# Kernel optimization log

Hardware: AMD Instinct MI355X
Metric: run time of the kernel (lower is better)

## Reference

```python
import jax, jax.numpy as jnp
import numpy as np

GROUP_SIZE = 128
HIDDEN = 2048
INTER = 5632
TOKENS = 8192
_SHIFTS = jnp.arange(8, dtype=jnp.uint32) * 4  # 4-bit nibbles, 8 per int32


def _pack_rows(nib):
    # nib: [in, out] int values in [0,16); pack 8 consecutive rows into one int32
    r, c = nib.shape
    n = nib.reshape(r // 8, 8, c).astype(jnp.uint32)
    packed = jnp.sum(n << _SHIFTS[None, :, None], axis=1, dtype=jnp.uint32)
    return jax.lax.bitcast_convert_type(packed, jnp.int32)  # [in//8, out]


def _pack_cols(nib):
    # nib: [groups, out]; pack 8 consecutive cols into one int32
    g, o = nib.shape
    n = nib.reshape(g, o // 8, 8).astype(jnp.uint32)
    packed = jnp.sum(n << _SHIFTS[None, None, :], axis=-1, dtype=jnp.uint32)
    return jax.lax.bitcast_convert_type(packed, jnp.int32)  # [groups, out//8]


def _dequant(qweight, qzeros, scales, group_size=GROUP_SIZE):
    # GPTQ int4 dequant: w = (q - (z + 1)) * scale, per group of `group_size` input rows
    in_packed, out = qweight.shape
    in_dim = in_packed * 8
    groups = scales.shape[0]
    sh = jnp.arange(8, dtype=jnp.int32) * 4
    q = (qweight[:, None, :] >> sh[None, :, None]) & 0xF       # [in//8, 8, out]
    q = q.reshape(in_dim, out)
    z = (qzeros[:, :, None] >> sh[None, None, :]) & 0xF        # [groups, out//8, 8]
    z = z.reshape(groups, out)
    gidx = jnp.arange(in_dim) // group_size                    # [in]
    w = (q - (z[gidx] + 1)).astype(scales.dtype) * scales[gidx]
    return w  # [in, out]


def setup_inputs() -> dict:
    key = jax.random.key(0)
    ks = jax.random.split(key, 10)
    x = jax.random.normal(ks[0], (TOKENS, HIDDEN), dtype=jnp.float32)

    def make(kq, kz, ksc, in_dim, out_dim):
        qn = jax.random.randint(kq, (in_dim, out_dim), 0, 16, dtype=jnp.int32)
        zn = jax.random.randint(kz, (in_dim // GROUP_SIZE, out_dim), 0, 16, dtype=jnp.int32)
        sc = jax.random.uniform(ksc, (in_dim // GROUP_SIZE, out_dim), jnp.float32, 1e-3, 2e-2)
        return _pack_rows(qn), _pack_cols(zn), sc

    gq, gz, gs = make(ks[1], ks[2], ks[3], HIDDEN, INTER)
    uq, uz, us = make(ks[4], ks[5], ks[6], HIDDEN, INTER)
    dq, dz, ds = make(ks[7], ks[8], ks[9], INTER, HIDDEN)
    return {
        "x": x,
        "gate_qweight": gq, "gate_qzeros": gz, "gate_scales": gs,
        "up_qweight": uq, "up_qzeros": uz, "up_scales": us,
        "down_qweight": dq, "down_qzeros": dz, "down_scales": ds,
    }


def reference(x, gate_qweight, gate_qzeros, gate_scales,
              up_qweight, up_qzeros, up_scales,
              down_qweight, down_qzeros, down_scales):
    wg = _dequant(gate_qweight, gate_qzeros, gate_scales)  # [H, I]
    wu = _dequant(up_qweight, up_qzeros, up_scales)        # [H, I]
    wd = _dequant(down_qweight, down_qzeros, down_scales)  # [I, H]
    # fused_gate_up: silu(x @ Wg) * (x @ Wu)
    h = jax.nn.silu(x @ wg) * (x @ wu)                     # [T, I]
    return h @ wd                                          # [T, H]
```

## Files before the change

### kernel.cpp

```cpp
#include <hip/hip_runtime.h>

#define TOKENS 8192
#define HIDDEN 2048
#define INTER  5632

typedef _Float16 f16x8 __attribute__((ext_vector_type(8)));
typedef _Float16 f16x2 __attribute__((ext_vector_type(2)));
typedef float    f32x4 __attribute__((ext_vector_type(4)));

__device__ __forceinline__ void async_copy16(const void* g, void* l) {
  __builtin_amdgcn_global_load_lds(
      (const __attribute__((address_space(1))) unsigned int*)g,
      (__attribute__((address_space(3))) unsigned int*)l, 16, 0, 0);
}

#define BAR   __builtin_amdgcn_s_barrier()
#define SB0   __builtin_amdgcn_sched_barrier(0)
#define LGKM0 do { asm volatile("s_waitcnt lgkmcnt(0)" ::: "memory"); SB0; } while (0)
#define WAITVM(n) asm volatile("s_waitcnt vmcnt(" #n ")" ::: "memory")
#define PRIO(x) __builtin_amdgcn_s_setprio(x)

__device__ __forceinline__ f16x8 dq8(unsigned int q, f16x2 s2, f16x2 c2) {
  union { unsigned int u[4]; f16x8 v; } r;
#pragma unroll
  for (int j = 0; j < 4; ++j) {
    const unsigned int t = ((q >> (4 * j)) & 0x000F000Fu) | 0x64006400u;
    f16x2 h = __builtin_bit_cast(f16x2, t);
    h = (h - c2) * s2;
    r.u[j] = __builtin_bit_cast(unsigned int, h);
  }
  return r.v;
}


__global__ __launch_bounds__(256)
void k_convert_x(const float* __restrict__ x, _Float16* __restrict__ xs) {
  __shared__ float lt[64 * 33];
  const int kb0  = blockIdx.x;
  const int mt32 = blockIdx.y;
  const int t    = threadIdx.x;

  const int m_l  = t >> 3;
  const int k4a  = t & 7;
  const float* row = x + (size_t)(mt32 * 32 + m_l) * HIDDEN + kb0 * 64;
#pragma unroll
  for (int h = 0; h < 2; ++h) {
    const int k4 = k4a + h * 8;
    const float4 f = *(const float4*)(row + k4 * 4);
    lt[(k4 * 4 + 0) * 33 + m_l] = f.x;
    lt[(k4 * 4 + 1) * 33 + m_l] = f.y;
    lt[(k4 * 4 + 2) * 33 + m_l] = f.z;
    lt[(k4 * 4 + 3) * 33 + m_l] = f.w;
  }
  __syncthreads();

  const int kb_l = t >> 5;
  const int m_o  = t & 31;
  const int P[8] = {0, 4, 1, 5, 2, 6, 3, 7};
  f16x8 v;
#pragma unroll
  for (int j = 0; j < 8; ++j)
    v[j] = (_Float16)lt[(kb_l * 8 + P[j]) * 33 + m_o];
  const int kb   = kb0 * 8 + kb_l;
  const int mt128 = mt32 >> 2;
  const int m128  = (mt32 & 3) * 32 + m_o;
  *(f16x8*)(xs + ((size_t)(mt128 * 256 + kb) * 128 + m128) * 8) = v;
}

__global__ void k_dequant(const unsigned int* __restrict__ qw,
                          const unsigned int* __restrict__ qz,
                          const float* __restrict__ sc,
                          _Float16* __restrict__ out, int N, int N8) {
  const int n  = blockIdx.x * 256 + threadIdx.x;
  const int k8 = blockIdx.y;
  const int g  = k8 >> 4;
  unsigned int q  = qw[(size_t)k8 * N + n];
  unsigned int zw = qz[(size_t)g * N8 + (n >> 3)];
  int   z1 = (int)((zw >> ((n & 7) * 4)) & 0xFu) + 1;
  float s  = sc[(size_t)g * N + n];
  f16x8 w;
#pragma unroll
  for (int j = 0; j < 8; ++j)
    w[j] = (_Float16)((float)((int)((q >> (4 * j)) & 0xFu) - z1) * s);
  *(f16x8*)(out + ((size_t)k8 * N + n) * 8) = w;
}

__global__ __launch_bounds__(256, 2)
void k_gemm_gateup(const _Float16* __restrict__ xs,
                   const unsigned int* __restrict__ gq,
                   const unsigned int* __restrict__ gz,
                   const float* __restrict__ gs,
                   const unsigned int* __restrict__ uq,
                   const unsigned int* __restrict__ uz,
                   const float* __restrict__ us,
                   _Float16* __restrict__ hs) {
  __shared__ _Float16 Al[8192];
  const int nt = blockIdx.x, mt = blockIdx.y;
  const int tid = threadIdx.x;
  const int wave = tid >> 6, lane = tid & 63;
  const int wm = wave >> 1, wn = wave & 1;
  const int row16 = lane >> 4, col = lane & 15;
  const int slot = wave * 4;

  const _Float16* gA = xs + (size_t)mt * 256 * 1024;

  int afo[4], ncol[4];
#pragma unroll
  for (int i = 0; i < 4; ++i) {
    afo[i]  = (row16 * 128 + wm * 64 + i * 16 + col) * 8;
    ncol[i] = nt * 128 + wn * 64 + i * 16 + col;
  }

  const f32x4 zero = {0.f, 0.f, 0.f, 0.f};
  f32x4 accg[4][4], accu[4][4];
#pragma unroll
  for (int i = 0; i < 4; ++i)
#pragma unroll
    for (int j = 0; j < 4; ++j) { accg[i][j] = zero; accu[i][j] = zero; }

  f16x2 sg2[4], cg2[4], su2[4], cu2[4];

  for (int kit = 0; kit < HIDDEN / 64; ++kit) {
    if ((kit & 1) == 0) {
      const int g = kit >> 1;
#pragma unroll
      for (int ni = 0; ni < 4; ++ni) {
        const int n = ncol[ni];
        const float        sgf = gs[(size_t)g * INTER + n];
        const float        suf = us[(size_t)g * INTER + n];
        const unsigned int zgw = gz[(size_t)g * (INTER / 8) + (n >> 3)];
        const unsigned int zuw = uz[(size_t)g * (INTER / 8) + (n >> 3)];
        const int z1g = (int)((zgw >> ((n & 7) * 4)) & 0xFu) + 1;
        const int z1u = (int)((zuw >> ((n & 7) * 4)) & 0xFu) + 1;
        const _Float16 shg = (_Float16)sgf, shu = (_Float16)suf;
        const _Float16 chg = (_Float16)(float)(1024 + z1g);
        const _Float16 chu = (_Float16)(float)(1024 + z1u);
        sg2[ni] = (f16x2){shg, shg}; cg2[ni] = (f16x2){chg, chg};
        su2[ni] = (f16x2){shu, shu}; cu2[ni] = (f16x2){chu, chu};
      }
    }

    unsigned int bqg[2][4], bqu[2][4];
#pragma unroll
    for (int ks = 0; ks < 2; ++ks) {
      const size_t ro = (size_t)((kit * 8 + ks * 4 + row16)) * INTER;
#pragma unroll
      for (int ni = 0; ni < 4; ++ni) {
        bqg[ks][ni] = gq[ro + ncol[ni]];
        bqu[ks][ni] = uq[ro + ncol[ni]];
      }
    }

    __syncthreads();
#pragma unroll
    for (int q = 0; q < 4; ++q) {
      const int c = (slot + q) * 64 + lane;
      async_copy16(gA + (size_t)kit * 8192 + (size_t)c * 8,
                   (char*)Al + (size_t)(slot + q) * 1024);
    }
    __syncthreads();

#pragma unroll
    for (int ks = 0; ks < 2; ++ks) {
      const int kadd = ks * 4096;
      f16x8 af[4], bg[4], bu[4];
#pragma unroll
      for (int i = 0; i < 4; ++i)
        af[i] = *(const f16x8*)(Al + kadd + afo[i]);
#pragma unroll
      for (int ni = 0; ni < 4; ++ni) {
        bg[ni] = dq8(bqg[ks][ni], sg2[ni], cg2[ni]);
        bu[ni] = dq8(bqu[ks][ni], su2[ni], cu2[ni]);
      }
#pragma unroll
      for (int mi = 0; mi < 4; ++mi)
#pragma unroll
        for (int ni = 0; ni < 4; ++ni) {
          accg[mi][ni] = __builtin_amdgcn_mfma_f32_16x16x32_f16(af[mi], bg[ni], accg[mi][ni], 0, 0, 0);
          accu[mi][ni] = __builtin_amdgcn_mfma_f32_16x16x32_f16(af[mi], bu[ni], accu[mi][ni], 0, 0, 0);
        }
    }
  }
#pragma unroll
  for (int mi = 0; mi < 4; ++mi)
#pragma unroll
    for (int ni = 0; ni < 4; ++ni) {
      const int kg = ncol[ni];
      const size_t base = (size_t)(mt * (INTER / 8) + (kg >> 3)) * 1024 + (kg & 7);
#pragma unroll
      for (int r = 0; r < 4; ++r) {
        float g = accg[mi][ni][r], u = accu[mi][ni][r];
        float h = g / (1.f + __expf(-g)) * u;
        const int ml = wm * 64 + mi * 16 + row16 * 4 + r;
        hs[base + (size_t)ml * 8] = (_Float16)h;
      }
    }
}

__global__ __launch_bounds__(512, 1)
void k_gemm_down(const _Float16* __restrict__ hs,
                 const _Float16* __restrict__ wd,
                 float* __restrict__ out) {
  extern __shared__ _Float16 lds[];
  _Float16* A0 = lds;
  _Float16* A1 = lds + 16384;
  _Float16* B0 = lds + 32768;
  _Float16* B1 = lds + 49152;

  const int bid  = blockIdx.x;
  const int wgid = (bid & 7) * 32 + (bid >> 3);
  const int nt = wgid >> 5, mt = wgid & 31;

  const int tid  = threadIdx.x;
  const int wave = tid >> 6, lane = tid & 63;
  const int wm = wave >> 2, wn = wave & 3;
  const int row16 = lane >> 4, col = lane & 15;

  int afo[8], bfo[4];
#pragma unroll
  for (int i = 0; i < 8; ++i)
    afo[i] = wm * 8192 + row16 * 1024 + (i * 16 + col) * 8;
#pragma unroll
  for (int i = 0; i < 4; ++i)
    bfo[i] = row16 * 2048 + (wn * 64 + i * 16 + col) * 8;

  const f32x4 zero = {0.f, 0.f, 0.f, 0.f};
  f32x4 acc[8][4];
#pragma unroll
  for (int i = 0; i < 8; ++i)
#pragma unroll
    for (int j = 0; j < 4; ++j) acc[i][j] = zero;

  f16x8 af[4][2], bf[4][2];

#define DN_LOAD_A(AP, mh) \
  _Pragma("unroll") for (int mi_ = 0; mi_ < 4; ++mi_) \
  _Pragma("unroll") for (int ks_ = 0; ks_ < 2; ++ks_) \
    af[mi_][ks_] = *(const f16x8*)((AP) + afo[(mh) * 4 + mi_] + ks_ * 4096);

#define DN_LOAD_B(BP, nh) \
  _Pragma("unroll") for (int ni_ = 0; ni_ < 2; ++ni_) \
  _Pragma("unroll") for (int ks_ = 0; ks_ < 2; ++ks_) \
    bf[(nh) * 2 + ni_][ks_] = *(const f16x8*)((BP) + bfo[(nh) * 2 + ni_] + ks_ * 8192);

#define DN_MFMA(mh, nh) \
  _Pragma("unroll") for (int mi_ = 0; mi_ < 4; ++mi_) \
  _Pragma("unroll") for (int ni_ = 0; ni_ < 2; ++ni_) \
  _Pragma("unroll") for (int ks_ = 0; ks_ < 2; ++ks_) \
    acc[(mh) * 4 + mi_][(nh) * 2 + ni_] = __builtin_amdgcn_mfma_f32_16x16x32_f16( \
        af[mi_][ks_], bf[(nh) * 2 + ni_][ks_], acc[(mh) * 4 + mi_][(nh) * 2 + ni_], 0, 0, 0);

#define DN_STAGE_A(AP, kt) do { const int kt_ = (kt); \
  _Pragma("unroll") for (int q_ = 0; q_ < 4; ++q_) { \
    const int i_ = q_ * 512 + tid; \
    async_copy16(hs + (size_t)(((2 * mt + (i_ >> 10)) * 704 + kt_ * 8 + ((i_ >> 7) & 7)) * 128 + (i_ & 127)) * 8, \
                 (char*)(AP) + q_ * 8192 + wave * 1024); } } while (0)

#define DN_STAGE_B(BP, kt) do { const int kt_ = (kt); \
  _Pragma("unroll") for (int q_ = 0; q_ < 4; ++q_) { \
    const int i_ = q_ * 512 + tid; \
    async_copy16(wd + (size_t)((kt_ * 8 + (i_ >> 8)) * HIDDEN + nt * 256 + (i_ & 255)) * 8, \
                 (char*)(BP) + q_ * 8192 + wave * 1024); } } while (0)

  DN_STAGE_B(B0, 0); DN_STAGE_A(A0, 0);
  DN_STAGE_B(B1, 1); DN_STAGE_A(A1, 1);
  WAITVM(8);
  BAR; SB0;

  for (int t2 = 0; t2 < 44; ++t2) {
    const int e2 = (2 * t2 + 2 < 88) ? 2 * t2 + 2 : 87;
    const int o2 = (2 * t2 + 3 < 88) ? 2 * t2 + 3 : 87;
    DN_LOAD_A(A0, 0); DN_LOAD_B(B0, 0);
    BAR; LGKM0; PRIO(1); DN_MFMA(0, 0); PRIO(0); BAR; SB0;
    DN_LOAD_B(B0, 1);
    BAR; LGKM0; PRIO(1); DN_MFMA(0, 1); PRIO(0); BAR; SB0;
    DN_LOAD_A(A0, 1); DN_STAGE_B(B0, e2);
    BAR; LGKM0; PRIO(1); DN_MFMA(1, 0); PRIO(0); BAR; SB0;
    DN_STAGE_A(A0, e2);
    BAR; LGKM0; PRIO(1); DN_MFMA(1, 1); PRIO(0); WAITVM(8); BAR; SB0;
    DN_LOAD_A(A1, 0); DN_LOAD_B(B1, 0);
    BAR; LGKM0; PRIO(1); DN_MFMA(0, 0); PRIO(0); BAR; SB0;
    DN_LOAD_B(B1, 1);
    BAR; LGKM0; PRIO(1); DN_MFMA(0, 1); PRIO(0); BAR; SB0;
    DN_LOAD_A(A1, 1); DN_STAGE_B(B1, o2);
    BAR; LGKM0; PRIO(1); DN_MFMA(1, 0); PRIO(0); BAR; SB0;
    DN_STAGE_A(A1, o2);
    BAR; LGKM0; PRIO(1); DN_MFMA(1, 1); PRIO(0); WAITVM(8); BAR; SB0;
  }
  WAITVM(0);

#pragma unroll
  for (int mi = 0; mi < 8; ++mi)
#pragma unroll
    for (int ni = 0; ni < 4; ++ni) {
      const int n = nt * 256 + wn * 64 + ni * 16 + col;
#pragma unroll
      for (int r = 0; r < 4; ++r) {
        const int m = mt * 256 + wm * 128 + mi * 16 + row16 * 4 + r;
        out[(size_t)m * HIDDEN + n] = acc[mi][ni][r];
      }
    }
#undef DN_LOAD_A
#undef DN_LOAD_B
#undef DN_MFMA
#undef DN_STAGE_A
#undef DN_STAGE_B
}

extern "C" void kernel_launch(void* const* d_in, const int* in_sizes, int n_in,
                              void* d_out, int out_size, void* d_ws, size_t ws_size,
                              hipStream_t stream) {
  (void)in_sizes; (void)n_in; (void)out_size; (void)ws_size;
  const float*        x  = (const float*)d_in[0];
  const unsigned int* gq = (const unsigned int*)d_in[1];
  const unsigned int* gz = (const unsigned int*)d_in[2];
  const float*        gs = (const float*)d_in[3];
  const unsigned int* uq = (const unsigned int*)d_in[4];
  const unsigned int* uz = (const unsigned int*)d_in[5];
  const float*        us = (const float*)d_in[6];
  const unsigned int* dq = (const unsigned int*)d_in[7];
  const unsigned int* dz = (const unsigned int*)d_in[8];
  const float*        ds = (const float*)d_in[9];
  float* out = (float*)d_out;

  char* ws = (char*)d_ws;
  _Float16* xs  = (_Float16*)ws;
  _Float16* wdd = (_Float16*)(ws + (size_t)TOKENS * HIDDEN * 2);
  _Float16* hs  = wdd + (size_t)INTER * HIDDEN;

  static bool attr_set = false;
  if (!attr_set) {
    hipFuncSetAttribute((const void*)k_gemm_down,
                        hipFuncAttributeMaxDynamicSharedMemorySize, 131072);
    attr_set = true;
  }

  k_convert_x<<<dim3(HIDDEN / 64, TOKENS / 32), 256, 0, stream>>>(x, xs);
  k_dequant<<<dim3(HIDDEN / 256, INTER / 8), 256, 0, stream>>>(dq, dz, ds, wdd, HIDDEN, HIDDEN / 8);
  k_gemm_gateup<<<dim3(INTER / 128, TOKENS / 128), 256, 0, stream>>>(
      xs, gq, gz, gs, uq, uz, us, hs);
  k_gemm_down<<<dim3(256), 512, 131072, stream>>>(hs, wdd, out);
}
```

Baseline: 761.7 us.

## Split gate and up projections across separate waves with LDS epilogue exchange

The gate/up GEMM block grows to 512 threads: four waves compute the gate projection and four the up projection, each covering all 128 rows and 32 columns. The K step doubles to one full quantization group per iteration, so scales and zeros load once per iteration. The up accumulators go through LDS as fp16 so the gate waves can apply SiLU and the product. The aim is more waves per CU and fewer accumulator registers per wave, at the cost of an extra LDS round trip, rounding the up result to fp16 before the multiply, and redundant A-fragment LDS reads across the two wave sets.

```diff
diff --git a/kernel.cpp b/kernel.cpp
--- a/kernel.cpp
+++ b/kernel.cpp
@@ -5,6 +5,7 @@
 #define INTER  5632
 
 typedef _Float16 f16x8 __attribute__((ext_vector_type(8)));
+typedef _Float16 f16x4 __attribute__((ext_vector_type(4)));
 typedef _Float16 f16x2 __attribute__((ext_vector_type(2)));
 typedef float    f32x4 __attribute__((ext_vector_type(4)));
 
@@ -24,7 +25,8 @@
   union { unsigned int u[4]; f16x8 v; } r;
 #pragma unroll
   for (int j = 0; j < 4; ++j) {
-    const unsigned int t = ((q >> (4 * j)) & 0x000F000Fu) | 0x64006400u;
+    const unsigned int qs = q >> (4 * j);
+    const unsigned int t  = (qs & 0x000F000Fu) | 0x64006400u;
     f16x2 h = __builtin_bit_cast(f16x2, t);
     h = (h - c2) * s2;
     r.u[j] = __builtin_bit_cast(unsigned int, h);
@@ -85,7 +87,7 @@
   *(f16x8*)(out + ((size_t)k8 * N + n) * 8) = w;
 }
 
-__global__ __launch_bounds__(256, 2)
+__global__ __launch_bounds__(512, 4)
 void k_gemm_gateup(const _Float16* __restrict__ xs,
                    const unsigned int* __restrict__ gq,
                    const unsigned int* __restrict__ gz,
@@ -94,107 +96,118 @@
                    const unsigned int* __restrict__ uz,
                    const float* __restrict__ us,
                    _Float16* __restrict__ hs) {
-  __shared__ _Float16 Al[8192];
+  __shared__ _Float16 smem[16384];
   const int nt = blockIdx.x, mt = blockIdx.y;
-  const int tid = threadIdx.x;
+  const int tid  = threadIdx.x;
   const int wave = tid >> 6, lane = tid & 63;
-  const int wm = wave >> 1, wn = wave & 1;
+  const int isUp = wave >> 2;
+  const int wg4  = wave & 3;
   const int row16 = lane >> 4, col = lane & 15;
-  const int slot = wave * 4;
+
+  const unsigned int* bq = isUp ? uq : gq;
+  const unsigned int* bz = isUp ? uz : gz;
+  const float*        bs = isUp ? us : gs;
+
+  int ncol[2];
+  ncol[0] = nt * 128 + wg4 * 32 + col;
+  ncol[1] = ncol[0] + 16;
+
+  int afo[8];
+#pragma unroll
+  for (int i = 0; i < 8; ++i)
+    afo[i] = (row16 * 128 + i * 16 + col) * 8;
 
   const _Float16* gA = xs + (size_t)mt * 256 * 1024;
 
-  int afo[4], ncol[4];
-#pragma unroll
-  for (int i = 0; i < 4; ++i) {
-    afo[i]  = (row16 * 128 + wm * 64 + i * 16 + col) * 8;
-    ncol[i] = nt * 128 + wn * 64 + i * 16 + col;
-  }
-
   const f32x4 zero = {0.f, 0.f, 0.f, 0.f};
-  f32x4 accg[4][4], accu[4][4];
-#pragma unroll
-  for (int i = 0; i < 4; ++i)
-#pragma unroll
-    for (int j = 0; j < 4; ++j) { accg[i][j] = zero; accu[i][j] = zero; }
-
-  f16x2 sg2[4], cg2[4], su2[4], cu2[4];
-
-  for (int kit = 0; kit < HIDDEN / 64; ++kit) {
-    if ((kit & 1) == 0) {
-      const int g = kit >> 1;
-#pragma unroll
-      for (int ni = 0; ni < 4; ++ni) {
-        const int n = ncol[ni];
-        const float        sgf = gs[(size_t)g * INTER + n];
-        const float        suf = us[(size_t)g * INTER + n];
-        const unsigned int zgw = gz[(size_t)g * (INTER / 8) + (n >> 3)];
-        const unsigned int zuw = uz[(size_t)g * (INTER / 8) + (n >> 3)];
-        const int z1g = (int)((zgw >> ((n & 7) * 4)) & 0xFu) + 1;
-        const int z1u = (int)((zuw >> ((n & 7) * 4)) & 0xFu) + 1;
-        const _Float16 shg = (_Float16)sgf, shu = (_Float16)suf;
-        const _Float16 chg = (_Float16)(float)(1024 + z1g);
-        const _Float16 chu = (_Float16)(float)(1024 + z1u);
-        sg2[ni] = (f16x2){shg, shg}; cg2[ni] = (f16x2){chg, chg};
-        su2[ni] = (f16x2){shu, shu}; cu2[ni] = (f16x2){chu, chu};
+  f32x4 acc[8][2];
+#pragma unroll
+  for (int i = 0; i < 8; ++i) { acc[i][0] = zero; acc[i][1] = zero; }
+
+  for (int kit = 0; kit < 16; ++kit) {
+    f16x2 s2[2], c2[2];
+#pragma unroll
+    for (int ni = 0; ni < 2; ++ni) {
+      const int n = ncol[ni];
+      const float        sf = bs[(size_t)kit * INTER + n];
+      const unsigned int zw = bz[(size_t)kit * (INTER / 8) + (n >> 3)];
+      const int z1 = (int)((zw >> ((n & 7) * 4)) & 0xFu) + 1;
+      const _Float16 sh = (_Float16)sf;
+      const _Float16 ch = (_Float16)(float)(1024 + z1);
+      s2[ni] = (f16x2){sh, sh};
+      c2[ni] = (f16x2){ch, ch};
+    }
+
+    unsigned int bqr[4][2];
+#pragma unroll
+    for (int ks = 0; ks < 4; ++ks) {
+      const size_t ro = (size_t)(kit * 16 + ks * 4 + row16) * INTER;
+      bqr[ks][0] = bq[ro + ncol[0]];
+      bqr[ks][1] = bq[ro + ncol[1]];
+    }
+
+    __syncthreads();
+#pragma unroll
+    for (int q = 0; q < 4; ++q) {
+      const int c = q * 512 + tid;
+      async_copy16(gA + (size_t)kit * 16384 + (size_t)c * 8, (char*)smem + (size_t)c * 16);
+    }
+    __syncthreads();
+
+#pragma unroll
+    for (int ks = 0; ks < 4; ++ks) {
+      f16x8 bf[2];
+      bf[0] = dq8(bqr[ks][0], s2[0], c2[0]);
+      bf[1] = dq8(bqr[ks][1], s2[1], c2[1]);
+#pragma unroll
+      for (int mh = 0; mh < 2; ++mh) {
+        f16x8 af[4];
+#pragma unroll
+        for (int i = 0; i < 4; ++i)
+          af[i] = *(const f16x8*)(smem + ks * 4096 + afo[mh * 4 + i]);
+#pragma unroll
+        for (int mi = 0; mi < 4; ++mi)
+#pragma unroll
+          for (int ni = 0; ni < 2; ++ni)
+            acc[mh * 4 + mi][ni] = __builtin_amdgcn_mfma_f32_16x16x32_f16(
+                af[mi], bf[ni], acc[mh * 4 + mi][ni], 0, 0, 0);
       }
     }
-
-    unsigned int bqg[2][4], bqu[2][4];
-#pragma unroll
-    for (int ks = 0; ks < 2; ++ks) {
-      const size_t ro = (size_t)((kit * 8 + ks * 4 + row16)) * INTER;
-#pragma unroll
-      for (int ni = 0; ni < 4; ++ni) {
-        bqg[ks][ni] = gq[ro + ncol[ni]];
-        bqu[ks][ni] = uq[ro + ncol[ni]];
+  }
+
+  __syncthreads();
+  if (isUp) {
+    _Float16* epi = smem;
+#pragma unroll
+    for (int mi = 0; mi < 8; ++mi)
+#pragma unroll
+      for (int ni = 0; ni < 2; ++ni) {
+        f16x4 u4;
+#pragma unroll
+        for (int r = 0; r < 4; ++r) u4[r] = (_Float16)acc[mi][ni][r];
+        *(f16x4*)(epi + (((size_t)wg4 * 16 + mi * 2 + ni) * 64 + lane) * 4) = u4;
       }
-    }
-
-    __syncthreads();
-#pragma unroll
-    for (int q = 0; q < 4; ++q) {
-      const int c = (slot + q) * 64 + lane;
-      async_copy16(gA + (size_t)kit * 8192 + (size_t)c * 8,
-                   (char*)Al + (size_t)(slot + q) * 1024);
-    }
-    __syncthreads();
-
-#pragma unroll
-    for (int ks = 0; ks < 2; ++ks) {
-      const int kadd = ks * 4096;
-      f16x8 af[4], bg[4], bu[4];
-#pragma unroll
-      for (int i = 0; i < 4; ++i)
-        af[i] = *(const f16x8*)(Al + kadd + afo[i]);
-#pragma unroll
-      for (int ni = 0; ni < 4; ++ni) {
-        bg[ni] = dq8(bqg[ks][ni], sg2[ni], cg2[ni]);
-        bu[ni] = dq8(bqu[ks][ni], su2[ni], cu2[ni]);
+  }
+  __syncthreads();
+  if (!isUp) {
+    const _Float16* epi = smem;
+#pragma unroll
+    for (int mi = 0; mi < 8; ++mi)
+#pragma unroll
+      for (int ni = 0; ni < 2; ++ni) {
+        const f16x4 u4 = *(const f16x4*)(epi + (((size_t)wg4 * 16 + mi * 2 + ni) * 64 + lane) * 4);
+        const int kg = ncol[ni];
+        const size_t base = (size_t)(mt * (INTER / 8) + (kg >> 3)) * 1024 + (kg & 7);
+#pragma unroll
+        for (int r = 0; r < 4; ++r) {
+          const float g = acc[mi][ni][r];
+          const float u = (float)u4[r];
+          const float h = g / (1.f + __expf(-g)) * u;
+          const int ml = mi * 16 + row16 * 4 + r;
+          hs[base + (size_t)ml * 8] = (_Float16)h;
+        }
       }
-#pragma unroll
-      for (int mi = 0; mi < 4; ++mi)
-#pragma unroll
-        for (int ni = 0; ni < 4; ++ni) {
-          accg[mi][ni] = __builtin_amdgcn_mfma_f32_16x16x32_f16(af[mi], bg[ni], accg[mi][ni], 0, 0, 0);
-          accu[mi][ni] = __builtin_amdgcn_mfma_f32_16x16x32_f16(af[mi], bu[ni], accu[mi][ni], 0, 0, 0);
-        }
-    }
-  }
-#pragma unroll
-  for (int mi = 0; mi < 4; ++mi)
-#pragma unroll
-    for (int ni = 0; ni < 4; ++ni) {
-      const int kg = ncol[ni];
-      const size_t base = (size_t)(mt * (INTER / 8) + (kg >> 3)) * 1024 + (kg & 7);
-#pragma unroll
-      for (int r = 0; r < 4; ++r) {
-        float g = accg[mi][ni][r], u = accu[mi][ni][r];
-        float h = g / (1.f + __expf(-g)) * u;
-        const int ml = wm * 64 + mi * 16 + row16 * 4 + r;
-        hs[base + (size_t)ml * 8] = (_Float16)h;
-      }
-    }
+  }
 }
 
 __global__ __launch_bounds__(512, 1)
@@ -337,7 +350,7 @@
 
   k_convert_x<<<dim3(HIDDEN / 64, TOKENS / 32), 256, 0, stream>>>(x, xs);
   k_dequant<<<dim3(HIDDEN / 256, INTER / 8), 256, 0, stream>>>(dq, dz, ds, wdd, HIDDEN, HIDDEN / 8);
-  k_gemm_gateup<<<dim3(INTER / 128, TOKENS / 128), 256, 0, stream>>>(
+  k_gemm_gateup<<<dim3(INTER / 128, TOKENS / 128), 512, 0, stream>>>(
       xs, gq, gz, gs, uq, uz, us, hs);
   k_gemm_down<<<dim3(256), 512, 131072, stream>>>(hs, wdd, out);
 }
```

After: 670.9 us. 1.14x faster.

## Pipeline gate/up GEMM with triple-buffered A, register-prefetched B, LDS-staged scales

Applied to the files above, without the earlier changes.

Restructures the fused gate/up int4 GEMM kernel into a software pipeline. The A tile goes through a three-slot LDS ring filled by async global-to-LDS copies two iterations ahead, and the packed weights are prefetched into registers two k-steps ahead. Scales and zeros for the whole tile are staged into LDS once at kernel start. The wave layout also changes so each wave covers all 128 rows by 32 columns instead of a 64x64 quadrant. This replaces two full barriers per iteration with a counted vmcnt wait plus one barrier, aiming to hide global load latency. The cost is more dynamic LDS (about 66 KB) and more registers, which may reduce occupancy below the declared two blocks per CU.

```diff
diff --git a/kernel.cpp b/kernel.cpp
--- a/kernel.cpp
+++ b/kernel.cpp
@@ -3,6 +3,7 @@
 #define TOKENS 8192
 #define HIDDEN 2048
 #define INTER  5632
+#define NKIT   32
 
 typedef _Float16 f16x8 __attribute__((ext_vector_type(8)));
 typedef _Float16 f16x2 __attribute__((ext_vector_type(2)));
@@ -12,6 +13,11 @@
   __builtin_amdgcn_global_load_lds(
       (const __attribute__((address_space(1))) unsigned int*)g,
       (__attribute__((address_space(3))) unsigned int*)l, 16, 0, 0);
+}
+__device__ __forceinline__ void async_copy4(const void* g, void* l) {
+  __builtin_amdgcn_global_load_lds(
+      (const __attribute__((address_space(1))) unsigned int*)g,
+      (__attribute__((address_space(3))) unsigned int*)l, 4, 0, 0);
 }
 
 #define BAR   __builtin_amdgcn_s_barrier()
@@ -94,107 +100,128 @@
                    const unsigned int* __restrict__ uz,
                    const float* __restrict__ us,
                    _Float16* __restrict__ hs) {
-  __shared__ _Float16 Al[8192];
+  extern __shared__ _Float16 lds[];
+  float*        scl = (float*)((char*)lds + 49152);
+  unsigned int* zer = (unsigned int*)((char*)lds + 65536);
+
   const int nt = blockIdx.x, mt = blockIdx.y;
-  const int tid = threadIdx.x;
+  const int tid  = threadIdx.x;
   const int wave = tid >> 6, lane = tid & 63;
-  const int wm = wave >> 1, wn = wave & 1;
+  const int wn = wave;
   const int row16 = lane >> 4, col = lane & 15;
-  const int slot = wave * 4;
-
-  const _Float16* gA = xs + (size_t)mt * 256 * 1024;
-
-  int afo[4], ncol[4];
-#pragma unroll
-  for (int i = 0; i < 4; ++i) {
-    afo[i]  = (row16 * 128 + wm * 64 + i * 16 + col) * 8;
-    ncol[i] = nt * 128 + wn * 64 + i * 16 + col;
-  }
+
+  const int ncol0 = nt * 128 + wn * 32 + col;
+  const int boff  = row16 * INTER + ncol0;
 
   const f32x4 zero = {0.f, 0.f, 0.f, 0.f};
-  f32x4 accg[4][4], accu[4][4];
-#pragma unroll
-  for (int i = 0; i < 4; ++i)
-#pragma unroll
-    for (int j = 0; j < 4; ++j) { accg[i][j] = zero; accu[i][j] = zero; }
-
-  f16x2 sg2[4], cg2[4], su2[4], cu2[4];
-
-  for (int kit = 0; kit < HIDDEN / 64; ++kit) {
-    if ((kit & 1) == 0) {
-      const int g = kit >> 1;
-#pragma unroll
-      for (int ni = 0; ni < 4; ++ni) {
-        const int n = ncol[ni];
-        const float        sgf = gs[(size_t)g * INTER + n];
-        const float        suf = us[(size_t)g * INTER + n];
-        const unsigned int zgw = gz[(size_t)g * (INTER / 8) + (n >> 3)];
-        const unsigned int zuw = uz[(size_t)g * (INTER / 8) + (n >> 3)];
-        const int z1g = (int)((zgw >> ((n & 7) * 4)) & 0xFu) + 1;
-        const int z1u = (int)((zuw >> ((n & 7) * 4)) & 0xFu) + 1;
-        const _Float16 shg = (_Float16)sgf, shu = (_Float16)suf;
-        const _Float16 chg = (_Float16)(float)(1024 + z1g);
-        const _Float16 chu = (_Float16)(float)(1024 + z1u);
-        sg2[ni] = (f16x2){shg, shg}; cg2[ni] = (f16x2){chg, chg};
-        su2[ni] = (f16x2){shu, shu}; cu2[ni] = (f16x2){chu, chu};
-      }
-    }
-
-    unsigned int bqg[2][4], bqu[2][4];
-#pragma unroll
-    for (int ks = 0; ks < 2; ++ks) {
-      const size_t ro = (size_t)((kit * 8 + ks * 4 + row16)) * INTER;
-#pragma unroll
-      for (int ni = 0; ni < 4; ++ni) {
-        bqg[ks][ni] = gq[ro + ncol[ni]];
-        bqu[ks][ni] = uq[ro + ncol[ni]];
-      }
-    }
-
-    __syncthreads();
-#pragma unroll
-    for (int q = 0; q < 4; ++q) {
-      const int c = (slot + q) * 64 + lane;
-      async_copy16(gA + (size_t)kit * 8192 + (size_t)c * 8,
-                   (char*)Al + (size_t)(slot + q) * 1024);
-    }
-    __syncthreads();
-
-#pragma unroll
-    for (int ks = 0; ks < 2; ++ks) {
-      const int kadd = ks * 4096;
-      f16x8 af[4], bg[4], bu[4];
-#pragma unroll
-      for (int i = 0; i < 4; ++i)
-        af[i] = *(const f16x8*)(Al + kadd + afo[i]);
-#pragma unroll
-      for (int ni = 0; ni < 4; ++ni) {
-        bg[ni] = dq8(bqg[ks][ni], sg2[ni], cg2[ni]);
-        bu[ni] = dq8(bqu[ks][ni], su2[ni], cu2[ni]);
-      }
-#pragma unroll
-      for (int mi = 0; mi < 4; ++mi)
-#pragma unroll
-        for (int ni = 0; ni < 4; ++ni) {
-          accg[mi][ni] = __builtin_amdgcn_mfma_f32_16x16x32_f16(af[mi], bg[ni], accg[mi][ni], 0, 0, 0);
-          accu[mi][ni] = __builtin_amdgcn_mfma_f32_16x16x32_f16(af[mi], bu[ni], accu[mi][ni], 0, 0, 0);
-        }
-    }
-  }
-#pragma unroll
-  for (int mi = 0; mi < 4; ++mi)
-#pragma unroll
-    for (int ni = 0; ni < 4; ++ni) {
-      const int kg = ncol[ni];
-      const size_t base = (size_t)(mt * (INTER / 8) + (kg >> 3)) * 1024 + (kg & 7);
+  f32x4 accg[8][2], accu[8][2];
+#pragma unroll
+  for (int i = 0; i < 8; ++i) {
+    accg[i][0] = zero; accg[i][1] = zero;
+    accu[i][0] = zero; accu[i][1] = zero;
+  }
+
+  unsigned int bqE[2][2][2], bqO[2][2][2];
+  f16x2 s2[2][2], c2[2][2];
+
+#define GU_LOADB(BQ, KT) do { const int kt_ = (KT); \
+  _Pragma("unroll") for (int ks_ = 0; ks_ < 2; ++ks_) { \
+    const int ro_ = (kt_ * 8 + ks_ * 4) * INTER + boff; \
+    BQ[0][0][ks_] = gq[ro_];      BQ[0][1][ks_] = gq[ro_ + 16]; \
+    BQ[1][0][ks_] = uq[ro_];      BQ[1][1][ks_] = uq[ro_ + 16]; \
+  } } while (0)
+
+#define GU_STAGE_A(BUFB, KT) do { const int kt_ = (KT); const int bb_ = (BUFB); \
+  _Pragma("unroll") for (int q_ = 0; q_ < 4; ++q_) { \
+    const int i_ = q_ * 256 + tid; \
+    async_copy16(xs + ((size_t)((mt * 256 + kt_ * 8 + (i_ >> 7)) * 128) + (i_ & 127)) * 8, \
+                 (char*)lds + bb_ * 16384 + q_ * 4096 + wave * 1024); \
+  } } while (0)
+
+#define GU_BUILDSC(G) do { const int g_ = (G); \
+  _Pragma("unroll") for (int mm_ = 0; mm_ < 2; ++mm_) \
+  _Pragma("unroll") for (int ni_ = 0; ni_ < 2; ++ni_) { \
+    const int cc_ = wn * 32 + ni_ * 16 + col; \
+    const float sf_ = scl[(mm_ * 16 + g_) * 128 + cc_]; \
+    const unsigned int zw_ = zer[(mm_ * 16 + g_) * 16 + (cc_ >> 3)]; \
+    const int z1_ = (int)((zw_ >> ((cc_ & 7) * 4)) & 0xFu) + 1; \
+    const _Float16 sh_ = (_Float16)sf_; \
+    const _Float16 ch_ = (_Float16)(float)(1024 + z1_); \
+    s2[mm_][ni_] = (f16x2){sh_, sh_}; c2[mm_][ni_] = (f16x2){ch_, ch_}; \
+  } } while (0)
+
+#define GU_KIT(K, BQ) do { \
+  if (((K) & 1) == 0) GU_BUILDSC((K) >> 1); \
+  f16x8 bf_[2][2][2]; \
+  _Pragma("unroll") for (int mm_ = 0; mm_ < 2; ++mm_) \
+  _Pragma("unroll") for (int ni_ = 0; ni_ < 2; ++ni_) \
+  _Pragma("unroll") for (int ks_ = 0; ks_ < 2; ++ks_) \
+    bf_[mm_][ni_][ks_] = dq8(BQ[mm_][ni_][ks_], s2[mm_][ni_], c2[mm_][ni_]); \
+  const int kn_ = ((K) + 2 < NKIT) ? (K) + 2 : NKIT - 1; \
+  GU_LOADB(BQ, kn_); \
+  GU_STAGE_A(stg, kn_); \
+  { const _Float16* ab_ = lds + cur * 8192; \
+    _Pragma("unroll") for (int ks_ = 0; ks_ < 2; ++ks_) { \
+      f16x8 af_[8]; \
+      _Pragma("unroll") for (int mi_ = 0; mi_ < 8; ++mi_) \
+        af_[mi_] = *(const f16x8*)(ab_ + ks_ * 4096 + (row16 * 128 + mi_ * 16 + col) * 8); \
+      _Pragma("unroll") for (int mi_ = 0; mi_ < 8; ++mi_) \
+      _Pragma("unroll") for (int ni_ = 0; ni_ < 2; ++ni_) { \
+        accg[mi_][ni_] = __builtin_amdgcn_mfma_f32_16x16x32_f16(af_[mi_], bf_[0][ni_][ks_], accg[mi_][ni_], 0, 0, 0); \
+        accu[mi_][ni_] = __builtin_amdgcn_mfma_f32_16x16x32_f16(af_[mi_], bf_[1][ni_][ks_], accu[mi_][ni_], 0, 0, 0); \
+      } \
+    } } \
+  WAITVM(12); BAR; SB0; \
+  cur = (cur == 2) ? 0 : cur + 1; \
+  stg = (stg == 2) ? 0 : stg + 1; \
+} while (0)
+
+#pragma unroll
+  for (int q = 0; q < 4; ++q) {
+    const int c = q * 256 + tid;
+    const float* sp = (q >> 1) ? us : gs;
+    const int g = (c >> 5) & 15;
+    async_copy16(sp + (size_t)g * INTER + nt * 128 + (c & 31) * 4,
+                 (char*)lds + 49152 + q * 4096 + wave * 1024);
+  }
+#pragma unroll
+  for (int q = 0; q < 2; ++q) {
+    const int c = q * 256 + tid;
+    const unsigned int* zp = q ? uz : gz;
+    const int g = (c >> 4) & 15;
+    async_copy4(zp + (size_t)g * (INTER / 8) + nt * 16 + (c & 15),
+                (char*)lds + 65536 + q * 1024 + wave * 256);
+  }
+  GU_LOADB(bqE, 0); GU_STAGE_A(0, 0);
+  GU_LOADB(bqO, 1); GU_STAGE_A(1, 1);
+  WAITVM(12);
+  BAR; SB0;
+
+  int cur = 0, stg = 2;
+  for (int k2 = 0; k2 < 16; ++k2) {
+    GU_KIT(2 * k2,     bqE);
+    GU_KIT(2 * k2 + 1, bqO);
+  }
+  WAITVM(0);
+
+#pragma unroll
+  for (int mi = 0; mi < 8; ++mi)
+#pragma unroll
+    for (int ni = 0; ni < 2; ++ni) {
+      const int kg = nt * 128 + wn * 32 + ni * 16 + col;
+      const size_t base = (size_t)(mt * 704 + (kg >> 3)) * 1024 + (kg & 7);
 #pragma unroll
       for (int r = 0; r < 4; ++r) {
-        float g = accg[mi][ni][r], u = accu[mi][ni][r];
-        float h = g / (1.f + __expf(-g)) * u;
-        const int ml = wm * 64 + mi * 16 + row16 * 4 + r;
+        const float g = accg[mi][ni][r], u = accu[mi][ni][r];
+        const float h = g / (1.f + __expf(-g)) * u;
+        const int ml = mi * 16 + row16 * 4 + r;
         hs[base + (size_t)ml * 8] = (_Float16)h;
       }
     }
+#undef GU_LOADB
+#undef GU_STAGE_A
+#undef GU_BUILDSC
+#undef GU_KIT
 }
 
 __global__ __launch_bounds__(512, 1)
@@ -330,6 +357,8 @@
 
   static bool attr_set = false;
   if (!attr_set) {
+    hipFuncSetAttribute((const void*)k_gemm_gateup,
+                        hipFuncAttributeMaxDynamicSharedMemorySize, 67584);
     hipFuncSetAttribute((const void*)k_gemm_down,
                         hipFuncAttributeMaxDynamicSharedMemorySize, 131072);
     attr_set = true;
@@ -337,7 +366,7 @@
 
   k_convert_x<<<dim3(HIDDEN / 64, TOKENS / 32), 256, 0, stream>>>(x, xs);
   k_dequant<<<dim3(HIDDEN / 256, INTER / 8), 256, 0, stream>>>(dq, dz, ds, wdd, HIDDEN, HIDDEN / 8);
-  k_gemm_gateup<<<dim3(INTER / 128, TOKENS / 128), 256, 0, stream>>>(
+  k_gemm_gateup<<<dim3(INTER / 128, TOKENS / 128), 256, 67584, stream>>>(
       xs, gq, gz, gs, uq, uz, us, hs);
   k_gemm_down<<<dim3(256), 512, 131072, stream>>>(hs, wdd, out);
 }
```

New measurement: 630.2 us. 1.21x faster.
